# Performance work log

Hardware: AMD Instinct MI355X
Metric: run time of the kernel (lower is better)

The kernel has to match this reference:

```python
import jax, jax.numpy as jnp
import numpy as np

N_WIDTH = 64
N_ORDER = 4
N_ELEMENTS = 64
N_NODES = N_ELEMENTS * N_ORDER + 1  # 257
N_SAMPLES = 4096
X_MIN = 0.0
X_MAX = 1.0


def _lagrange(x, n_order):
    # x: [S, W] reference coords in [-1, 1] -> [S, W, P] basis values
    nodes = np.linspace(-1.0, 1.0, n_order + 1)
    cols = []
    for j in range(n_order + 1):
        p = jnp.ones_like(x)
        for m in range(n_order + 1):
            if m != j:
                p = p * (x - nodes[m]) / (nodes[j] - nodes[m])
        cols.append(p)
    return jnp.stack(cols, axis=-1)


def _dlagrange(x, n_order):
    nodes = np.linspace(-1.0, 1.0, n_order + 1)
    cols = []
    for j in range(n_order + 1):
        y = jnp.zeros_like(x)
        for i in range(n_order + 1):
            if i != j:
                k = jnp.full_like(x, 1.0 / (nodes[j] - nodes[i]))
                for m in range(n_order + 1):
                    if m != i and m != j:
                        k = k * (x - nodes[m]) / (nodes[j] - nodes[m])
                y = y + k
        cols.append(y)
    return jnp.stack(cols, axis=-1)


def _ddlagrange(x, n_order):
    nodes = np.linspace(-1.0, 1.0, n_order + 1)
    cols = []
    for j in range(n_order + 1):
        y = jnp.zeros_like(x)
        for i in range(n_order + 1):
            if i != j:
                k_sum = jnp.zeros_like(x)
                for m in range(n_order + 1):
                    if m != i and m != j:
                        k_prod = jnp.full_like(x, 1.0 / (nodes[j] - nodes[m]))
                        for n in range(n_order + 1):
                            if n != i and n != j and n != m:
                                k_prod = k_prod * (x - nodes[n]) / (nodes[j] - nodes[n])
                        k_sum = k_sum + k_prod
                y = y + k_sum / (nodes[j] - nodes[i])
        cols.append(y)
    return jnp.stack(cols, axis=-1)


def setup_inputs() -> dict:
    key = jax.random.key(0)
    k1, k2 = jax.random.split(key)
    x = jax.random.uniform(k1, (N_SAMPLES,), minval=X_MIN, maxval=X_MAX, dtype=jnp.float32)
    # xavier_normal_ for [n_width, n_nodes]: std = sqrt(2 / (fan_in + fan_out))
    std = np.sqrt(2.0 / (N_WIDTH + N_NODES)).astype(np.float32)
    weight = jax.random.normal(k2, (N_WIDTH, N_NODES), dtype=jnp.float32) * std
    return {"x": x, "weight": weight}


def reference(x, weight):
    if x.ndim != 2:
        x = jnp.repeat(x[:, None], N_WIDTH, axis=-1)  # [S, W]
    S = x.shape[0]
    x_shift = (N_NODES - 1) * (x - X_MIN) / (X_MAX - X_MIN)
    id_el = jnp.clip(jnp.floor(x_shift / N_ORDER), 0, N_ELEMENTS - 1)
    nodes_in_l = (id_el * N_ORDER).astype(jnp.int32)  # [S, W]
    # to_ref with node_r - node_l == n_order
    x_t = 2.0 * (x_shift - nodes_in_l) / N_ORDER - 1.0
    delta_x = 0.5 * N_ORDER * (X_MAX - X_MIN) / (N_NODES - 1)

    phi_l = _lagrange(x_t, N_ORDER)                       # [S, W, P]
    dphi_l = _dlagrange(x_t, N_ORDER) / delta_x
    ddphi_l = _ddlagrange(x_t, N_ORDER) / (delta_x ** 2)

    P = N_ORDER + 1
    idx = nodes_in_l[:, :, None] + jnp.arange(P)          # [S, W, P] global node ids
    si = jnp.arange(S)[:, None, None]
    wi = jnp.arange(N_WIDTH)[None, :, None]

    def scatter(vals):
        return jnp.zeros((S, N_WIDTH, N_NODES), vals.dtype).at[si, wi, idx].set(vals)

    phi_ikp = scatter(phi_l)
    dphi_ikp = scatter(dphi_l)
    ddphi_ikp = scatter(ddphi_l)

    t_ik = jnp.einsum('kp,ikp->ik', weight, phi_ikp)
    dt_ik = jnp.einsum('kp,ikp->ik', weight, dphi_ikp)
    ddt_ik = jnp.einsum('kp,ikp->ik', weight, ddphi_ikp)
    return (t_ik, dt_ik, ddt_ik, phi_ikp, dphi_ikp, ddphi_ikp, jnp.float32(delta_x))
```

## Files before the change

### kernel.cpp

```cpp
#include <hip/hip_runtime.h>

#define NS     4096
#define NW     64
#define NNODES 257
#define SW     (NS * NW)
#define ROW    (NW * NNODES)
#define ROW4   (ROW / 4)
#define SWN    ((size_t)NS * NW * NNODES)

__device__ __constant__ const float P4[5] = { (float)( 2.0/3.0), (float)(-8.0/3.0),  4.0f, (float)(-8.0/3.0), (float)( 2.0/3.0) };
__device__ __constant__ const float P3[5] = { (float)(-2.0/3.0), (float)( 4.0/3.0),  0.0f, (float)(-4.0/3.0), (float)( 2.0/3.0) };
__device__ __constant__ const float P2[5] = { (float)(-1.0/6.0), (float)( 8.0/3.0), -5.0f, (float)( 8.0/3.0), (float)(-1.0/6.0) };
__device__ __constant__ const float P1[5] = { (float)( 1.0/6.0), (float)(-4.0/3.0),  0.0f, (float)( 4.0/3.0), (float)(-1.0/6.0) };
__device__ __constant__ const float P0[5] = { 0.0f, 0.0f, 1.0f, 0.0f, 0.0f };

__device__ __constant__ const float D3[5] = { (float)( 1024.0/3.0), (float)(-4096.0/3.0),  2048.0f, (float)(-4096.0/3.0), (float)(1024.0/3.0) };
__device__ __constant__ const float D2[5] = { -256.0f, 512.0f, 0.0f, -512.0f, 256.0f };
__device__ __constant__ const float D1[5] = { (float)( -128.0/3.0), (float)( 2048.0/3.0), -1280.0f, (float)( 2048.0/3.0), (float)(-128.0/3.0) };
__device__ __constant__ const float D0[5] = { (float)(   64.0/3.0), (float)( -512.0/3.0),     0.0f, (float)(  512.0/3.0), (float)( -64.0/3.0) };

__device__ __constant__ const float E2[5] = { 131072.0f, -524288.0f, 786432.0f, -524288.0f, 131072.0f };
__device__ __constant__ const float E1[5] = { -65536.0f,  131072.0f,      0.0f, -131072.0f,  65536.0f };
__device__ __constant__ const float E0[5] = { (float)(-16384.0/3.0), (float)(262144.0/3.0), -163840.0f, (float)(262144.0/3.0), (float)(-16384.0/3.0) };

__global__ __launch_bounds__(256) void kann_all(
    const float* __restrict__ x,
    const float* __restrict__ weight,
    float* __restrict__ out)
{
    const int i   = blockIdx.x;
    const int tid = threadIdx.x;

    const float xs = 256.0f * x[i];
    float fel = floorf(xs * 0.25f);
    fel = fminf(fmaxf(fel, 0.0f), 63.0f);
    const int   b = (int)fel * 4;
    const float t = 0.5f * (xs - (float)b) - 1.0f;

    float bas[3][5];
    #pragma unroll
    for (int j = 0; j < 5; ++j) {
        bas[0][j] = (((P4[j]*t + P3[j])*t + P2[j])*t + P1[j])*t + P0[j];
        bas[1][j] = ((D3[j]*t + D2[j])*t + D1[j])*t + D0[j];
        bas[2][j] = (E2[j]*t + E1[j])*t + E0[j];
    }

    if (tid < NW) {
        const float* wrow = weight + tid * NNODES + b;
        float s0 = 0.0f, s1 = 0.0f, s2 = 0.0f;
        #pragma unroll
        for (int j = 0; j < 5; ++j) {
            const float w = wrow[j];
            s0 += w * bas[0][j];
            s1 += w * bas[1][j];
            s2 += w * bas[2][j];
        }
        out[(size_t)i * NW + tid]                   = s0;
        out[SW + (size_t)i * NW + tid]              = s1;
        out[2 * (size_t)SW + (size_t)i * NW + tid]  = s2;
    }
    if (i == 0 && tid == 64)
        out[3 * (size_t)SW + 3 * SWN] = 0.0078125f;

    const int g0 = b >> 2;
    int h0 = -1, h1 = -1;
    float w0v[3][4], w1v[3][4];
    #pragma unroll
    for (int a = 0; a < 3; ++a)
        #pragma unroll
        for (int c = 0; c < 4; ++c) { w0v[a][c] = 0.0f; w1v[a][c] = 0.0f; }

    #pragma unroll
    for (int rho = 0; rho < 4; ++rho) {
        #pragma unroll
        for (int p = 0; p < 2; ++p) {
            const int gm = 64 * rho + g0 + p;
            int d = tid - gm;
            if (d < 0) d += 257;
            if (d < 17) {
                h1 = h0;
                #pragma unroll
                for (int a = 0; a < 3; ++a)
                    #pragma unroll
                    for (int c = 0; c < 4; ++c) w1v[a][c] = w0v[a][c];
                h0 = d;
                #pragma unroll
                for (int a = 0; a < 3; ++a) {
                    #pragma unroll
                    for (int c = 0; c < 4; ++c) {
                        const int j = 4 * p + c - rho;
                        w0v[a][c] = (j >= 0 && j <= 4) ? bas[a][j] : 0.0f;
                    }
                }
            }
        }
    }

    float* big = out + 3 * (size_t)SW + (size_t)i * ROW;
    float4* r0 = reinterpret_cast<float4*>(big);
    float4* r1 = reinterpret_cast<float4*>(big + SWN);
    float4* r2 = reinterpret_cast<float4*>(big + 2 * SWN);

    #pragma unroll
    for (int n = 0; n < 16; ++n) {
        const int o = tid + (n << 8);
        float v[3][4];
        #pragma unroll
        for (int a = 0; a < 3; ++a) {
            #pragma unroll
            for (int c = 0; c < 4; ++c) {
                const float t1 = (n == h1) ? w1v[a][c] : 0.0f;
                v[a][c]        = (n == h0) ? w0v[a][c] : t1;
            }
        }
        r0[o] = make_float4(v[0][0], v[0][1], v[0][2], v[0][3]);
        r1[o] = make_float4(v[1][0], v[1][1], v[1][2], v[1][3]);
        r2[o] = make_float4(v[2][0], v[2][1], v[2][2], v[2][3]);
    }

    if (tid < 16) {
        const int n = 16;
        const int o = tid + (n << 8);
        float v[3][4];
        #pragma unroll
        for (int a = 0; a < 3; ++a) {
            #pragma unroll
            for (int c = 0; c < 4; ++c) {
                const float t1 = (n == h1) ? w1v[a][c] : 0.0f;
                v[a][c]        = (n == h0) ? w0v[a][c] : t1;
            }
        }
        r0[o] = make_float4(v[0][0], v[0][1], v[0][2], v[0][3]);
        r1[o] = make_float4(v[1][0], v[1][1], v[1][2], v[1][3]);
        r2[o] = make_float4(v[2][0], v[2][1], v[2][2], v[2][3]);
    }
}

extern "C" void kernel_launch(void* const* d_in, const int* in_sizes, int n_in,
                              void* d_out, int out_size, void* d_ws, size_t ws_size,
                              hipStream_t stream) {
    const float* x      = (const float*)d_in[0];
    const float* weight = (const float*)d_in[1];
    float* out          = (float*)d_out;
    kann_all<<<NS, 256, 0, stream>>>(x, weight, out);
}
```

Before: 153.6 us.

## Split fused kernel into basis, scatter-write, and dot kernels with nontemporal stores

Replaces the single fused kernel with three launches. The first precomputes basis values per sample into the workspace. The second writes each of the three large scattered tensors in its own block using nontemporal vector stores. The third computes the small dot products with four samples per block. The aim is lower register pressure and better store streaming, at the cost of extra launches and a workspace round trip; the old kernel remains as a fallback when the workspace is too small.

```diff
diff --git a/kernel.cpp b/kernel.cpp
--- a/kernel.cpp
+++ b/kernel.cpp
@@ -8,6 +8,8 @@
 #define ROW4   (ROW / 4)
 #define SWN    ((size_t)NS * NW * NNODES)
 
+typedef float v4f __attribute__((ext_vector_type(4)));
+
 __device__ __constant__ const float P4[5] = { (float)( 2.0/3.0), (float)(-8.0/3.0),  4.0f, (float)(-8.0/3.0), (float)( 2.0/3.0) };
 __device__ __constant__ const float P3[5] = { (float)(-2.0/3.0), (float)( 4.0/3.0),  0.0f, (float)(-4.0/3.0), (float)( 2.0/3.0) };
 __device__ __constant__ const float P2[5] = { (float)(-1.0/6.0), (float)( 8.0/3.0), -5.0f, (float)( 8.0/3.0), (float)(-1.0/6.0) };
@@ -23,53 +25,55 @@
 __device__ __constant__ const float E1[5] = { -65536.0f,  131072.0f,      0.0f, -131072.0f,  65536.0f };
 __device__ __constant__ const float E0[5] = { (float)(-16384.0/3.0), (float)(262144.0/3.0), -163840.0f, (float)(262144.0/3.0), (float)(-16384.0/3.0) };
 
-__global__ __launch_bounds__(256) void kann_all(
-    const float* __restrict__ x,
-    const float* __restrict__ weight,
-    float* __restrict__ out)
-{
-    const int i   = blockIdx.x;
-    const int tid = threadIdx.x;
-
-    const float xs = 256.0f * x[i];
+__device__ __forceinline__ void basis_all(float xi, int* b_out, float bas[3][5])
+{
+    const float xs = 256.0f * xi;
     float fel = floorf(xs * 0.25f);
     fel = fminf(fmaxf(fel, 0.0f), 63.0f);
     const int   b = (int)fel * 4;
     const float t = 0.5f * (xs - (float)b) - 1.0f;
-
-    float bas[3][5];
     #pragma unroll
     for (int j = 0; j < 5; ++j) {
         bas[0][j] = (((P4[j]*t + P3[j])*t + P2[j])*t + P1[j])*t + P0[j];
         bas[1][j] = ((D3[j]*t + D2[j])*t + D1[j])*t + D0[j];
         bas[2][j] = (E2[j]*t + E1[j])*t + E0[j];
     }
-
-    if (tid < NW) {
-        const float* wrow = weight + tid * NNODES + b;
-        float s0 = 0.0f, s1 = 0.0f, s2 = 0.0f;
-        #pragma unroll
-        for (int j = 0; j < 5; ++j) {
-            const float w = wrow[j];
-            s0 += w * bas[0][j];
-            s1 += w * bas[1][j];
-            s2 += w * bas[2][j];
-        }
-        out[(size_t)i * NW + tid]                   = s0;
-        out[SW + (size_t)i * NW + tid]              = s1;
-        out[2 * (size_t)SW + (size_t)i * NW + tid]  = s2;
-    }
-    if (i == 0 && tid == 64)
-        out[3 * (size_t)SW + 3 * SWN] = 0.0078125f;
-
+    *b_out = b;
+}
+
+__global__ __launch_bounds__(256) void k_basis(
+    const float* __restrict__ x, float* __restrict__ ws)
+{
+    const int i = blockIdx.x * 256 + threadIdx.x;
+    if (i >= NS) return;
+    int b; float bas[3][5];
+    basis_all(x[i], &b, bas);
+    float* r = ws + (size_t)i * 16;
+    #pragma unroll
+    for (int j = 0; j < 5; ++j) {
+        r[j]      = bas[0][j];
+        r[5 + j]  = bas[1][j];
+        r[10 + j] = bas[2][j];
+    }
+    r[15] = (float)b;
+}
+
+__global__ __launch_bounds__(256) void k_write(
+    const float* __restrict__ ws, float* __restrict__ out)
+{
+    const int i   = blockIdx.x;
+    const int a   = blockIdx.y;
+    const int tid = threadIdx.x;
+
+    const float* tb = ws + (size_t)i * 16;
+    float ba[5];
+    #pragma unroll
+    for (int j = 0; j < 5; ++j) ba[j] = tb[a * 5 + j];
+    const int b  = (int)tb[15];
     const int g0 = b >> 2;
+
     int h0 = -1, h1 = -1;
-    float w0v[3][4], w1v[3][4];
-    #pragma unroll
-    for (int a = 0; a < 3; ++a)
-        #pragma unroll
-        for (int c = 0; c < 4; ++c) { w0v[a][c] = 0.0f; w1v[a][c] = 0.0f; }
-
+    float w0[4] = {0.f,0.f,0.f,0.f}, w1[4] = {0.f,0.f,0.f,0.f};
     #pragma unroll
     for (int rho = 0; rho < 4; ++rho) {
         #pragma unroll
@@ -80,56 +84,159 @@
             if (d < 17) {
                 h1 = h0;
                 #pragma unroll
+                for (int c = 0; c < 4; ++c) w1[c] = w0[c];
+                h0 = d;
+                #pragma unroll
+                for (int c = 0; c < 4; ++c) {
+                    const int j = 4 * p + c - rho;
+                    w0[c] = (j >= 0 && j <= 4) ? ba[j] : 0.0f;
+                }
+            }
+        }
+    }
+
+    v4f* r = reinterpret_cast<v4f*>(
+        out + 3 * (size_t)SW + (size_t)a * SWN + (size_t)i * ROW);
+
+    #pragma unroll
+    for (int n = 0; n < 16; ++n) {
+        const int o = tid + (n << 8);
+        float v[4];
+        #pragma unroll
+        for (int c = 0; c < 4; ++c) {
+            const float t1 = (n == h1) ? w1[c] : 0.0f;
+            v[c]           = (n == h0) ? w0[c] : t1;
+        }
+        const v4f val = { v[0], v[1], v[2], v[3] };
+        __builtin_nontemporal_store(val, &r[o]);
+    }
+    if (tid < 16) {
+        const int n = 16;
+        const int o = tid + (n << 8);
+        float v[4];
+        #pragma unroll
+        for (int c = 0; c < 4; ++c) {
+            const float t1 = (n == h1) ? w1[c] : 0.0f;
+            v[c]           = (n == h0) ? w0[c] : t1;
+        }
+        const v4f val = { v[0], v[1], v[2], v[3] };
+        __builtin_nontemporal_store(val, &r[o]);
+    }
+}
+
+__global__ __launch_bounds__(256) void k_dots(
+    const float* __restrict__ ws, const float* __restrict__ weight,
+    float* __restrict__ out)
+{
+    const int tid  = threadIdx.x;
+    const int lane = tid & 63;
+    const int i    = blockIdx.x * 4 + (tid >> 6);
+
+    const float* tb = ws + (size_t)i * 16;
+    const int b = (int)tb[15];
+    const float* wrow = weight + lane * NNODES + b;
+
+    float s0 = 0.0f, s1 = 0.0f, s2 = 0.0f;
+    #pragma unroll
+    for (int j = 0; j < 5; ++j) {
+        const float w = wrow[j];
+        s0 += w * tb[j];
+        s1 += w * tb[5 + j];
+        s2 += w * tb[10 + j];
+    }
+    out[(size_t)i * NW + lane]                  = s0;
+    out[SW + (size_t)i * NW + lane]             = s1;
+    out[2 * (size_t)SW + (size_t)i * NW + lane] = s2;
+
+    if (blockIdx.x == 0 && tid == 0)
+        out[3 * (size_t)SW + 3 * SWN] = 0.0078125f;
+}
+
+__global__ __launch_bounds__(256) void kann_all(
+    const float* __restrict__ x, const float* __restrict__ weight,
+    float* __restrict__ out)
+{
+    const int i   = blockIdx.x;
+    const int tid = threadIdx.x;
+
+    int b; float bas[3][5];
+    basis_all(x[i], &b, bas);
+
+    if (tid < NW) {
+        const float* wrow = weight + tid * NNODES + b;
+        float s0 = 0.0f, s1 = 0.0f, s2 = 0.0f;
+        #pragma unroll
+        for (int j = 0; j < 5; ++j) {
+            const float w = wrow[j];
+            s0 += w * bas[0][j]; s1 += w * bas[1][j]; s2 += w * bas[2][j];
+        }
+        out[(size_t)i * NW + tid]                  = s0;
+        out[SW + (size_t)i * NW + tid]             = s1;
+        out[2 * (size_t)SW + (size_t)i * NW + tid] = s2;
+    }
+    if (i == 0 && tid == 64) out[3 * (size_t)SW + 3 * SWN] = 0.0078125f;
+
+    const int g0 = b >> 2;
+    int h0 = -1, h1 = -1;
+    float w0v[3][4], w1v[3][4];
+    #pragma unroll
+    for (int a = 0; a < 3; ++a)
+        #pragma unroll
+        for (int c = 0; c < 4; ++c) { w0v[a][c] = 0.0f; w1v[a][c] = 0.0f; }
+    #pragma unroll
+    for (int rho = 0; rho < 4; ++rho) {
+        #pragma unroll
+        for (int p = 0; p < 2; ++p) {
+            const int gm = 64 * rho + g0 + p;
+            int d = tid - gm;
+            if (d < 0) d += 257;
+            if (d < 17) {
+                h1 = h0;
+                #pragma unroll
                 for (int a = 0; a < 3; ++a)
                     #pragma unroll
                     for (int c = 0; c < 4; ++c) w1v[a][c] = w0v[a][c];
                 h0 = d;
                 #pragma unroll
-                for (int a = 0; a < 3; ++a) {
+                for (int a = 0; a < 3; ++a)
                     #pragma unroll
                     for (int c = 0; c < 4; ++c) {
                         const int j = 4 * p + c - rho;
                         w0v[a][c] = (j >= 0 && j <= 4) ? bas[a][j] : 0.0f;
                     }
-                }
-            }
-        }
-    }
-
+            }
+        }
+    }
     float* big = out + 3 * (size_t)SW + (size_t)i * ROW;
     float4* r0 = reinterpret_cast<float4*>(big);
     float4* r1 = reinterpret_cast<float4*>(big + SWN);
     float4* r2 = reinterpret_cast<float4*>(big + 2 * SWN);
-
     #pragma unroll
     for (int n = 0; n < 16; ++n) {
         const int o = tid + (n << 8);
         float v[3][4];
         #pragma unroll
-        for (int a = 0; a < 3; ++a) {
+        for (int a = 0; a < 3; ++a)
             #pragma unroll
             for (int c = 0; c < 4; ++c) {
                 const float t1 = (n == h1) ? w1v[a][c] : 0.0f;
                 v[a][c]        = (n == h0) ? w0v[a][c] : t1;
             }
-        }
         r0[o] = make_float4(v[0][0], v[0][1], v[0][2], v[0][3]);
         r1[o] = make_float4(v[1][0], v[1][1], v[1][2], v[1][3]);
         r2[o] = make_float4(v[2][0], v[2][1], v[2][2], v[2][3]);
     }
-
     if (tid < 16) {
         const int n = 16;
         const int o = tid + (n << 8);
         float v[3][4];
         #pragma unroll
-        for (int a = 0; a < 3; ++a) {
+        for (int a = 0; a < 3; ++a)
             #pragma unroll
             for (int c = 0; c < 4; ++c) {
                 const float t1 = (n == h1) ? w1v[a][c] : 0.0f;
                 v[a][c]        = (n == h0) ? w0v[a][c] : t1;
             }
-        }
         r0[o] = make_float4(v[0][0], v[0][1], v[0][2], v[0][3]);
         r1[o] = make_float4(v[1][0], v[1][1], v[1][2], v[1][3]);
         r2[o] = make_float4(v[2][0], v[2][1], v[2][2], v[2][3]);
@@ -142,5 +249,14 @@
     const float* x      = (const float*)d_in[0];
     const float* weight = (const float*)d_in[1];
     float* out          = (float*)d_out;
-    kann_all<<<NS, 256, 0, stream>>>(x, weight, out);
-}
+
+    if (ws_size >= (size_t)NS * 16 * sizeof(float)) {
+        float* ws = (float*)d_ws;
+        k_basis<<<NS / 256, 256, 0, stream>>>(x, ws);
+        dim3 g(NS, 3);
+        k_write<<<g, 256, 0, stream>>>(ws, out);
+        k_dots<<<NS / 4, 256, 0, stream>>>(ws, weight, out);
+    } else {
+        kann_all<<<NS, 256, 0, stream>>>(x, weight, out);
+    }
+}
```

Measured after the change: 173.3 us. 1.13x slower.
